# Performance work log

Hardware: AMD Instinct MI355X
Metric: run time of the kernel (lower is better)

## Reference

```python
import jax, jax.numpy as jnp
import numpy as np

N_NODES = 100000
D_FEAT = 128
K_NEIGH = 16
N_LAYERS = 2
F_OUT = 128  # features = [128, 128]


def setup_inputs() -> dict:
    key = jax.random.key(0)
    k1, k2, k3 = jax.random.split(key, 3)
    feats = jax.random.normal(k1, (N_NODES, D_FEAT), dtype=jnp.float32)
    # per-layer sampled neighbor indices (fresh sampling each layer, as in the source)
    neigh_idx = jax.random.randint(k2, (N_LAYERS, N_NODES, K_NEIGH), 0, N_NODES, dtype=jnp.int32)
    # Dense kernels: input is concat(self, mean_neighbors) -> 2*D; both layers 256 -> 128
    Ws = jax.random.normal(k3, (N_LAYERS, 2 * D_FEAT, F_OUT), dtype=jnp.float32) * (1.0 / np.sqrt(2 * D_FEAT))
    bs = jnp.zeros((N_LAYERS, F_OUT), dtype=jnp.float32)
    return {"feats": feats, "neigh_idx": neigh_idx, "Ws": Ws, "bs": bs}


def reference(feats, neigh_idx, Ws, bs):
    """GraphSAGE (mean aggregator): per layer, gather sampled neighbors,
    mean-aggregate, concat with self, Dense; relu between layers.
    Returns the last-layer Dense output (pre-relu), matching `new_feats`
    returned by the source module.
    """
    h = feats  # [N, D]
    z = h
    for l in range(Ws.shape[0]):
        neigh = h[neigh_idx[l]]              # [N, K, D] irregular gather
        agg = neigh.mean(axis=1)             # [N, D] mean aggregation
        cat = jnp.concatenate([h, agg], axis=-1)  # [N, 2D]
        z = cat @ Ws[l] + bs[l]              # [N, F]
        h = jax.nn.relu(z)
    return z
```

## Files before the change

kernel.cpp:

```cpp
#include <hip/hip_runtime.h>

#define N_NODES 100000
#define D 128
#define K 16
#define MB 16

typedef __attribute__((ext_vector_type(8))) short bf16x8;
typedef __attribute__((ext_vector_type(4))) float f32x4;
typedef __attribute__((ext_vector_type(2))) float f32x2;

#define LDS_BYTES 38208

__device__ __forceinline__ unsigned short f2bf(float f) {
    union { float f; unsigned u; } v; v.f = f;
    unsigned u = v.u;
    return (unsigned short)((u + 0x7fffu + ((u >> 16) & 1u)) >> 16);
}
__device__ __forceinline__ unsigned pk4(float a, float b, float c, float d) {
    int w = __builtin_amdgcn_cvt_pk_fp8_f32(a, b, 0, false);
    w = __builtin_amdgcn_cvt_pk_fp8_f32(c, d, w, true);
    return (unsigned)w;
}

__global__ void cvt_all(const float* __restrict__ feats, const float* __restrict__ Ws,
                        unsigned* __restrict__ f8, unsigned short* __restrict__ Wt,
                        unsigned char* __restrict__ W8) {
    int tid = blockIdx.x * 256 + threadIdx.x;
    int i = tid * 16;
    if (i < N_NODES * D) {
        const float4* p = (const float4*)(feats + i);
        float4 v0 = p[0], v1 = p[1], v2 = p[2], v3 = p[3];
        uint4 o;
        o.x = pk4(v0.x, v0.y, v0.z, v0.w);
        o.y = pk4(v1.x, v1.y, v1.z, v1.w);
        o.z = pk4(v2.x, v2.y, v2.z, v2.w);
        o.w = pk4(v3.x, v3.y, v3.z, v3.w);
        *(uint4*)(f8 + i / 4) = o;
    }
    if (tid < 2 * D * D) {
        int l = tid >> 14, r = tid & 16383;
        int n = r >> 7, k = r & 127;
        const float* Wl = Ws + l * (2 * D * D);
        Wt[tid] = f2bf(Wl[k * D + n]);
        int w = __builtin_amdgcn_cvt_pk_fp8_f32(Wl[(D + k) * D + n] * 16.f, 0.f, 0, false);
        W8[tid] = (unsigned char)(w & 0xff);
    }
}

template <int LAYER>
__launch_bounds__(256, 4)
__global__ void sage_layer(const float* __restrict__ self_f32,
                           const unsigned short* __restrict__ self_bf,
                           const unsigned char* __restrict__ g8,
                           const int* __restrict__ idx,
                           const unsigned short* __restrict__ Wt,
                           const unsigned char* __restrict__ W8,
                           const float* __restrict__ bias,
                           unsigned short* __restrict__ h_out,
                           unsigned char* __restrict__ h8_out,
                           float* __restrict__ z_out) {
    __shared__ __align__(16) char sm[LDS_BYTES];
    unsigned short (*sSelf)[136] = (unsigned short (*)[136])(sm + 32768);
    int (*sIdx)[17] = (int (*)[17])(sm + 37120);
    float (*zb)[132] = (float (*)[132])sm;

    const int t = threadIdx.x;
    const int base = blockIdx.x * MB;
    const int lane = t & 63;
    const int wave = t >> 6;
    const int q = lane >> 4;
    const int nlo = lane & 15;

    sIdx[t >> 4][t & 15] = idx[(size_t)base * K + t];

    {
        int m = t >> 4, c = (t & 15) * 8;
        if (LAYER == 0) {
            const float4* sp = (const float4*)(self_f32 + (size_t)(base + m) * D + c);
            float4 a = sp[0], b = sp[1];
            unsigned w0 = (unsigned)f2bf(a.x) | ((unsigned)f2bf(a.y) << 16);
            unsigned w1 = (unsigned)f2bf(a.z) | ((unsigned)f2bf(a.w) << 16);
            unsigned w2 = (unsigned)f2bf(b.x) | ((unsigned)f2bf(b.y) << 16);
            unsigned w3 = (unsigned)f2bf(b.z) | ((unsigned)f2bf(b.w) << 16);
            *(uint4*)&sSelf[m][c] = make_uint4(w0, w1, w2, w3);
        } else {
            *(uint4*)&sSelf[m][c] = *(const uint4*)(self_bf + (size_t)(base + m) * D + c);
        }
    }
    __syncthreads();

#pragma unroll
    for (int nn = 0; nn < 4; ++nn) {
        int n = wave * 4 + nn;
#pragma unroll
        for (int j = 0; j < 2; ++j) {
            int m = j * 8 + (lane >> 3);
            int node = sIdx[m][n];
            int c = (((lane & 7) - m) << 4) & 127;
            const void* gp = (const void*)(g8 + ((size_t)node << 7) + c);
            void* lp = (void*)(sm + n * 2048 + j * 1024);
            __builtin_amdgcn_global_load_lds(
                (const __attribute__((address_space(1))) unsigned int*)gp,
                (__attribute__((address_space(3))) unsigned int*)lp, 16, 0, 0);
        }
    }

    long b8[2][4];
    bf16x8 bsf[2][4];
#pragma unroll
    for (int nt = 0; nt < 2; ++nt) {
        int col = wave * 32 + nt * 16 + nlo;
#pragma unroll
        for (int ksm = 0; ksm < 4; ++ksm) {
            b8[nt][ksm] = *(const long*)(W8 + (size_t)col * 128 + ksm * 32 + q * 8);
            bsf[nt][ksm] = *(const bf16x8*)(Wt + (size_t)col * 128 + ksm * 32 + q * 8);
        }
    }

    __syncthreads();

    f32x4 aAgg0 = {}, aAgg1 = {}, aSelf0 = {}, aSelf1 = {};
#pragma unroll 8
    for (int ks = 0; ks < 64; ++ks) {
        int n = ks >> 2, ksm = ks & 3;
        int ro = (ksm * 32 + q * 8 + nlo * 16) & 127;
        long av = *(const long*)(sm + n * 2048 + nlo * 128 + ro);
        aAgg0 = __builtin_amdgcn_mfma_f32_16x16x32_fp8_fp8(av, b8[0][ksm], aAgg0, 0, 0, 0);
        aAgg1 = __builtin_amdgcn_mfma_f32_16x16x32_fp8_fp8(av, b8[1][ksm], aAgg1, 0, 0, 0);
    }
#pragma unroll
    for (int ks = 0; ks < 4; ++ks) {
        bf16x8 av = *(const bf16x8*)&sSelf[nlo][ks * 32 + q * 8];
        aSelf0 = __builtin_amdgcn_mfma_f32_16x16x32_bf16(av, bsf[0][ks], aSelf0, 0, 0, 0);
        aSelf1 = __builtin_amdgcn_mfma_f32_16x16x32_bf16(av, bsf[1][ks], aSelf1, 0, 0, 0);
    }

    __syncthreads();
#pragma unroll
    for (int nt = 0; nt < 2; ++nt) {
        int col = wave * 32 + nt * 16 + nlo;
        float bv = bias[col];
        f32x4 vs = nt ? aSelf1 : aSelf0;
        f32x4 va = nt ? aAgg1 : aAgg0;
#pragma unroll
        for (int r = 0; r < 4; ++r)
            zb[q * 4 + r][col] = vs[r] + va[r] * (1.0f / 256.0f) + bv;
    }
    __syncthreads();
    {
        int m = t >> 4, c = (t & 15) * 8;
        float x[8];
        *(f32x4*)&x[0] = *(const f32x4*)&zb[m][c];
        *(f32x4*)&x[4] = *(const f32x4*)&zb[m][c + 4];
        size_t go = (size_t)(base + m) * D + c;
        if (LAYER == 1) {
            float4* zp = (float4*)(z_out + go);
            zp[0] = make_float4(x[0], x[1], x[2], x[3]);
            zp[1] = make_float4(x[4], x[5], x[6], x[7]);
        } else {
#pragma unroll
            for (int i = 0; i < 8; ++i) x[i] = x[i] > 0.f ? x[i] : 0.f;
            unsigned w0 = (unsigned)f2bf(x[0]) | ((unsigned)f2bf(x[1]) << 16);
            unsigned w1 = (unsigned)f2bf(x[2]) | ((unsigned)f2bf(x[3]) << 16);
            unsigned w2 = (unsigned)f2bf(x[4]) | ((unsigned)f2bf(x[5]) << 16);
            unsigned w3 = (unsigned)f2bf(x[6]) | ((unsigned)f2bf(x[7]) << 16);
            *(uint4*)(h_out + go) = make_uint4(w0, w1, w2, w3);
            uint2 o8;
            o8.x = pk4(x[0], x[1], x[2], x[3]);
            o8.y = pk4(x[4], x[5], x[6], x[7]);
            *(uint2*)(h8_out + go) = o8;
        }
    }
}

extern "C" void kernel_launch(void* const* d_in, const int* in_sizes, int n_in,
                              void* d_out, int out_size, void* d_ws, size_t ws_size,
                              hipStream_t stream) {
    const float* feats = (const float*)d_in[0];
    const int* neigh   = (const int*)d_in[1];
    const float* Ws    = (const float*)d_in[2];
    const float* bs    = (const float*)d_in[3];
    float* out = (float*)d_out;

    char* ws = (char*)d_ws;
    unsigned short* h1_bf  = (unsigned short*)(ws);
    unsigned char*  feats8 = (unsigned char*)(ws + 25600000);
    unsigned char*  h18    = (unsigned char*)(ws + 38400000);
    unsigned short* Wt     = (unsigned short*)(ws + 51200000);
    unsigned char*  W8     = (unsigned char*)(ws + 51265536);

    cvt_all<<<3125, 256, 0, stream>>>(feats, Ws, (unsigned*)feats8, Wt, W8);

    sage_layer<0><<<N_NODES / MB, 256, 0, stream>>>(
        feats, nullptr, feats8, neigh, Wt, W8, bs, h1_bf, h18, nullptr);
    sage_layer<1><<<N_NODES / MB, 256, 0, stream>>>(
        nullptr, h1_bf, h18, neigh + N_NODES * K, Wt + D * D, W8 + D * D, bs + D,
        nullptr, nullptr, out);
}
```

Before: 237.0 us.

## Pre-aggregate neighbor mean in registers, then single bf16 MFMA over concatenated K=256

```diff
diff --git a/kernel.cpp b/kernel.cpp
--- a/kernel.cpp
+++ b/kernel.cpp
@@ -3,13 +3,14 @@
 #define N_NODES 100000
 #define D 128
 #define K 16
+#define CATK 256
 #define MB 16
 
 typedef __attribute__((ext_vector_type(8))) short bf16x8;
 typedef __attribute__((ext_vector_type(4))) float f32x4;
 typedef __attribute__((ext_vector_type(2))) float f32x2;
 
-#define LDS_BYTES 38208
+#define LDS_BYTES 41216
 
 __device__ __forceinline__ unsigned short f2bf(float f) {
     union { float f; unsigned u; } v; v.f = f;
@@ -21,10 +22,14 @@
     w = __builtin_amdgcn_cvt_pk_fp8_f32(c, d, w, true);
     return (unsigned)w;
 }
+__device__ __forceinline__ void dec4(unsigned w, float* acc) {
+    f32x2 lo = __builtin_amdgcn_cvt_pk_f32_fp8((int)w, false);
+    f32x2 hi = __builtin_amdgcn_cvt_pk_f32_fp8((int)w, true);
+    acc[0] += lo.x; acc[1] += lo.y; acc[2] += hi.x; acc[3] += hi.y;
+}
 
 __global__ void cvt_all(const float* __restrict__ feats, const float* __restrict__ Ws,
-                        unsigned* __restrict__ f8, unsigned short* __restrict__ Wt,
-                        unsigned char* __restrict__ W8) {
+                        unsigned* __restrict__ f8, unsigned short* __restrict__ Wt) {
     int tid = blockIdx.x * 256 + threadIdx.x;
     int i = tid * 16;
     if (i < N_NODES * D) {
@@ -37,32 +42,28 @@
         o.w = pk4(v3.x, v3.y, v3.z, v3.w);
         *(uint4*)(f8 + i / 4) = o;
     }
-    if (tid < 2 * D * D) {
-        int l = tid >> 14, r = tid & 16383;
-        int n = r >> 7, k = r & 127;
-        const float* Wl = Ws + l * (2 * D * D);
-        Wt[tid] = f2bf(Wl[k * D + n]);
-        int w = __builtin_amdgcn_cvt_pk_fp8_f32(Wl[(D + k) * D + n] * 16.f, 0.f, 0, false);
-        W8[tid] = (unsigned char)(w & 0xff);
+    if (tid < 2 * CATK * D) {
+        int l = tid / (CATK * D);
+        int r = tid % (CATK * D);
+        int n = r / CATK, k = r % CATK;
+        Wt[tid] = f2bf(Ws[l * CATK * D + k * D + n]);
     }
 }
 
 template <int LAYER>
-__launch_bounds__(256, 4)
+__launch_bounds__(256, 3)
 __global__ void sage_layer(const float* __restrict__ self_f32,
                            const unsigned short* __restrict__ self_bf,
                            const unsigned char* __restrict__ g8,
                            const int* __restrict__ idx,
                            const unsigned short* __restrict__ Wt,
-                           const unsigned char* __restrict__ W8,
                            const float* __restrict__ bias,
                            unsigned short* __restrict__ h_out,
                            unsigned char* __restrict__ h8_out,
                            float* __restrict__ z_out) {
     __shared__ __align__(16) char sm[LDS_BYTES];
-    unsigned short (*sSelf)[136] = (unsigned short (*)[136])(sm + 32768);
-    int (*sIdx)[17] = (int (*)[17])(sm + 37120);
-    float (*zb)[132] = (float (*)[132])sm;
+    unsigned short (*cat)[264] = (unsigned short (*)[264])(sm + 32768);
+    float (*zb)[132] = (float (*)[132])(sm + 32768);
 
     const int t = threadIdx.x;
     const int base = blockIdx.x * MB;
@@ -70,69 +71,78 @@
     const int wave = t >> 6;
     const int q = lane >> 4;
     const int nlo = lane & 15;
-
-    sIdx[t >> 4][t & 15] = idx[(size_t)base * K + t];
-
-    {
-        int m = t >> 4, c = (t & 15) * 8;
-        if (LAYER == 0) {
-            const float4* sp = (const float4*)(self_f32 + (size_t)(base + m) * D + c);
-            float4 a = sp[0], b = sp[1];
-            unsigned w0 = (unsigned)f2bf(a.x) | ((unsigned)f2bf(a.y) << 16);
-            unsigned w1 = (unsigned)f2bf(a.z) | ((unsigned)f2bf(a.w) << 16);
-            unsigned w2 = (unsigned)f2bf(b.x) | ((unsigned)f2bf(b.y) << 16);
-            unsigned w3 = (unsigned)f2bf(b.z) | ((unsigned)f2bf(b.w) << 16);
-            *(uint4*)&sSelf[m][c] = make_uint4(w0, w1, w2, w3);
-        } else {
-            *(uint4*)&sSelf[m][c] = *(const uint4*)(self_bf + (size_t)(base + m) * D + c);
-        }
-    }
-    __syncthreads();
-
-#pragma unroll
-    for (int nn = 0; nn < 4; ++nn) {
-        int n = wave * 4 + nn;
+    const int m = t >> 4;
+    const int c = (t & 15) * 8;
+
+    int vidx[8];
+#pragma unroll
+    for (int nn = 0; nn < 4; ++nn)
+#pragma unroll
+        for (int j = 0; j < 2; ++j)
+            vidx[nn * 2 + j] =
+                idx[(size_t)(base + j * 8 + (lane >> 3)) * K + wave * 4 + nn];
+
+    bf16x8 bfrag[2][8];
+#pragma unroll
+    for (int nt = 0; nt < 2; ++nt) {
+        int col = wave * 32 + nt * 16 + nlo;
+        const unsigned short* wp = Wt + (size_t)col * CATK + q * 8;
+#pragma unroll
+        for (int ks = 0; ks < 8; ++ks)
+            bfrag[nt][ks] = *(const bf16x8*)(wp + ks * 32);
+    }
+
+#pragma unroll
+    for (int nn = 0; nn < 4; ++nn)
 #pragma unroll
         for (int j = 0; j < 2; ++j) {
-            int m = j * 8 + (lane >> 3);
-            int node = sIdx[m][n];
-            int c = (((lane & 7) - m) << 4) & 127;
-            const void* gp = (const void*)(g8 + ((size_t)node << 7) + c);
-            void* lp = (void*)(sm + n * 2048 + j * 1024);
+            int node = vidx[nn * 2 + j];
+            const void* gp = (const void*)(g8 + ((size_t)node << 7) + ((lane & 7) << 4));
+            void* lp = (void*)(sm + (wave * 4 + nn) * 2048 + j * 1024);
             __builtin_amdgcn_global_load_lds(
                 (const __attribute__((address_space(1))) unsigned int*)gp,
                 (__attribute__((address_space(3))) unsigned int*)lp, 16, 0, 0);
         }
-    }
-
-    long b8[2][4];
-    bf16x8 bsf[2][4];
-#pragma unroll
-    for (int nt = 0; nt < 2; ++nt) {
-        int col = wave * 32 + nt * 16 + nlo;
-#pragma unroll
-        for (int ksm = 0; ksm < 4; ++ksm) {
-            b8[nt][ksm] = *(const long*)(W8 + (size_t)col * 128 + ksm * 32 + q * 8);
-            bsf[nt][ksm] = *(const bf16x8*)(Wt + (size_t)col * 128 + ksm * 32 + q * 8);
+
+    if (LAYER == 0) {
+        const float4* sp = (const float4*)(self_f32 + (size_t)(base + m) * D + c);
+        float4 a = sp[0], b = sp[1];
+        unsigned w0 = (unsigned)f2bf(a.x) | ((unsigned)f2bf(a.y) << 16);
+        unsigned w1 = (unsigned)f2bf(a.z) | ((unsigned)f2bf(a.w) << 16);
+        unsigned w2 = (unsigned)f2bf(b.x) | ((unsigned)f2bf(b.y) << 16);
+        unsigned w3 = (unsigned)f2bf(b.z) | ((unsigned)f2bf(b.w) << 16);
+        *(uint4*)&cat[m][c] = make_uint4(w0, w1, w2, w3);
+    } else {
+        *(uint4*)&cat[m][c] = *(const uint4*)(self_bf + (size_t)(base + m) * D + c);
+    }
+
+    __syncthreads();
+
+    {
+        float acc[8];
+#pragma unroll
+        for (int i = 0; i < 8; ++i) acc[i] = 0.f;
+#pragma unroll
+        for (int k = 0; k < K; ++k) {
+            uint2 v = *(const uint2*)(sm + k * 2048 + m * 128 + c);
+            dec4(v.x, acc);
+            dec4(v.y, acc + 4);
         }
-    }
-
-    __syncthreads();
-
-    f32x4 aAgg0 = {}, aAgg1 = {}, aSelf0 = {}, aSelf1 = {};
-#pragma unroll 8
-    for (int ks = 0; ks < 64; ++ks) {
-        int n = ks >> 2, ksm = ks & 3;
-        int ro = (ksm * 32 + q * 8 + nlo * 16) & 127;
-        long av = *(const long*)(sm + n * 2048 + nlo * 128 + ro);
-        aAgg0 = __builtin_amdgcn_mfma_f32_16x16x32_fp8_fp8(av, b8[0][ksm], aAgg0, 0, 0, 0);
-        aAgg1 = __builtin_amdgcn_mfma_f32_16x16x32_fp8_fp8(av, b8[1][ksm], aAgg1, 0, 0, 0);
-    }
-#pragma unroll
-    for (int ks = 0; ks < 4; ++ks) {
-        bf16x8 av = *(const bf16x8*)&sSelf[nlo][ks * 32 + q * 8];
-        aSelf0 = __builtin_amdgcn_mfma_f32_16x16x32_bf16(av, bsf[0][ks], aSelf0, 0, 0, 0);
-        aSelf1 = __builtin_amdgcn_mfma_f32_16x16x32_bf16(av, bsf[1][ks], aSelf1, 0, 0, 0);
+        unsigned pk[4];
+#pragma unroll
+        for (int j = 0; j < 4; ++j)
+            pk[j] = (unsigned)f2bf(acc[2 * j] * (1.f / 16.f)) |
+                    ((unsigned)f2bf(acc[2 * j + 1] * (1.f / 16.f)) << 16);
+        *(uint4*)&cat[m][D + c] = make_uint4(pk[0], pk[1], pk[2], pk[3]);
+    }
+    __syncthreads();
+
+    f32x4 acc0 = {}, acc1 = {};
+#pragma unroll
+    for (int ks = 0; ks < 8; ++ks) {
+        bf16x8 av = *(const bf16x8*)&cat[nlo][ks * 32 + q * 8];
+        acc0 = __builtin_amdgcn_mfma_f32_16x16x32_bf16(av, bfrag[0][ks], acc0, 0, 0, 0);
+        acc1 = __builtin_amdgcn_mfma_f32_16x16x32_bf16(av, bfrag[1][ks], acc1, 0, 0, 0);
     }
 
     __syncthreads();
@@ -140,15 +150,13 @@
     for (int nt = 0; nt < 2; ++nt) {
         int col = wave * 32 + nt * 16 + nlo;
         float bv = bias[col];
-        f32x4 vs = nt ? aSelf1 : aSelf0;
-        f32x4 va = nt ? aAgg1 : aAgg0;
+        f32x4 va = nt ? acc1 : acc0;
 #pragma unroll
         for (int r = 0; r < 4; ++r)
-            zb[q * 4 + r][col] = vs[r] + va[r] * (1.0f / 256.0f) + bv;
+            zb[q * 4 + r][col] = va[r] + bv;
     }
     __syncthreads();
     {
-        int m = t >> 4, c = (t & 15) * 8;
         float x[8];
         *(f32x4*)&x[0] = *(const f32x4*)&zb[m][c];
         *(f32x4*)&x[4] = *(const f32x4*)&zb[m][c + 4];
@@ -187,13 +195,12 @@
     unsigned char*  feats8 = (unsigned char*)(ws + 25600000);
     unsigned char*  h18    = (unsigned char*)(ws + 38400000);
     unsigned short* Wt     = (unsigned short*)(ws + 51200000);
-    unsigned char*  W8     = (unsigned char*)(ws + 51265536);
-
-    cvt_all<<<3125, 256, 0, stream>>>(feats, Ws, (unsigned*)feats8, Wt, W8);
+
+    cvt_all<<<3125, 256, 0, stream>>>(feats, Ws, (unsigned*)feats8, Wt);
 
     sage_layer<0><<<N_NODES / MB, 256, 0, stream>>>(
-        feats, nullptr, feats8, neigh, Wt, W8, bs, h1_bf, h18, nullptr);
+        feats, nullptr, feats8, neigh, Wt, bs, h1_bf, h18, nullptr);
     sage_layer<1><<<N_NODES / MB, 256, 0, stream>>>(
-        nullptr, h1_bf, h18, neigh + N_NODES * K, Wt + D * D, W8 + D * D, bs + D,
+        nullptr, h1_bf, h18, neigh + N_NODES * K, Wt + CATK * D, bs + D,
         nullptr, nullptr, out);
 }
```

Result: no change. 234.8 us (-0.9%).
